# Optimization experiments

Measured on AMD Instinct MI355X. Metric: run time of the kernel, lower is better.

Reference implementation:

```python
import jax, jax.numpy as jnp
import numpy as np

TAU = 1.5
SCALE = 0.125
EPS = 1e-5
H = 8

@jax.custom_vjp
def spike(u):
    return (u >= 0.0).astype(u.dtype)

def _spike_fwd(u):
    return spike(u), u

def _spike_bwd(u, g):
    # ATan surrogate gradient, alpha=2 (spikingjelly default)
    return (g / (1.0 + (jnp.pi * u) ** 2),)

spike.defvjp(_spike_fwd, _spike_bwd)

def lif_ms(xt):
    # xt: (T, ...) multi-step LIF, decay_input=True, v_th=1, hard reset to 0, detach_reset
    def step(v, x):
        v = v + (x - v) / TAU
        s = spike(v - 1.0)
        v = v * (1.0 - jax.lax.stop_gradient(s))
        return v, s
    _, s = jax.lax.scan(step, jnp.zeros_like(xt[0]), xt)
    return s

def bn(x, g, b, m, var):
    # eval-mode BatchNorm1d over channel dim of (B, C, L)
    inv = g / jnp.sqrt(var + EPS)
    return (x - m[None, :, None]) * inv[None, :, None] + b[None, :, None]

def setup_inputs() -> dict:
    key = jax.random.key(0)
    ks = jax.random.split(key, 16)
    B, C, T, N = 8, 512, 4, 256
    w_scale = 1.0 / np.sqrt(C)
    inp = {
        'x': jax.random.normal(ks[0], (B, C, T, N), jnp.float32),
        'wq': jax.random.normal(ks[1], (C, C), jnp.float32) * w_scale,
        'wk': jax.random.normal(ks[2], (C, C), jnp.float32) * w_scale,
        'wv': jax.random.normal(ks[3], (C, C), jnp.float32) * w_scale,
        'wp': jax.random.normal(ks[4], (C, C), jnp.float32) * w_scale,
        'bp': jnp.zeros((C,), jnp.float32),
        'gq': jax.random.uniform(ks[5], (C,), jnp.float32, 0.5, 1.5),
        'bq': jax.random.uniform(ks[6], (C,), jnp.float32),
        'mq': jnp.zeros((C,), jnp.float32),
        'vq': jnp.ones((C,), jnp.float32),
        'gk': jax.random.uniform(ks[7], (C,), jnp.float32, 0.5, 1.5),
        'bk': jax.random.uniform(ks[8], (C,), jnp.float32),
        'mk': jnp.zeros((C,), jnp.float32),
        'vk': jnp.ones((C,), jnp.float32),
        'gv': jax.random.uniform(ks[9], (C,), jnp.float32, 0.5, 1.5),
        'bv': jax.random.uniform(ks[10], (C,), jnp.float32),
        'mv': jnp.zeros((C,), jnp.float32),
        'vv': jnp.ones((C,), jnp.float32),
        'gp': jax.random.uniform(ks[11], (C,), jnp.float32, 0.5, 1.5),
        'bpn': jax.random.uniform(ks[12], (C,), jnp.float32),
        'mp': jnp.zeros((C,), jnp.float32),
        'vp': jnp.ones((C,), jnp.float32),
    }
    return inp

def reference(x, wq, wk, wv, wp, bp, gq, bq, mq, vq, gk, bk, mk, vk,
              gv, bv, mv, vv, gp, bpn, mp, vp):
    B, C, T, N = x.shape
    L = T * N
    d = C // H

    # proj_bn then multi-step proj_lif over time dim
    xb = bn(x.reshape(B, C, L), gp, bpn, mp, vp).reshape(B, C, T, N)
    s0 = lif_ms(jnp.transpose(xb, (2, 0, 1, 3)))            # (T,B,C,N)
    x_for_qkv = jnp.transpose(s0, (1, 2, 0, 3)).reshape(B, C, L)  # (B,C,L)

    def qkv_branch(w, g, b_, m, v_):
        y = bn(jnp.einsum('oc,bcl->bol', w, x_for_qkv), g, b_, m, v_)
        y = y.reshape(B, C, T, N)
        sy = lif_ms(jnp.transpose(y, (2, 0, 1, 3)))         # (T,B,C,N)
        sy = jnp.transpose(sy, (1, 0, 3, 2)).reshape(B, L, C)  # (B,T,N,C)->(B,L,C)
        return jnp.transpose(sy.reshape(B, L, H, d), (0, 2, 1, 3))  # (B,H,L,d)

    q = qkv_branch(wq, gq, bq, mq, vq)
    k = qkv_branch(wk, gk, bk, mk, vk)
    v = qkv_branch(wv, gv, bv, mv, vv)

    attn = jnp.einsum('bhqd,bhkd->bhqk', q, k)              # no softmax
    o = jnp.einsum('bhqk,bhkd->bhqd', attn, v) * SCALE
    o = jnp.transpose(o, (0, 1, 3, 2)).reshape(B, C, L)

    # single-step attn_lif: v = o/tau from zero state, spike at threshold 1
    s = spike(o / TAU - 1.0)

    out = jnp.einsum('oc,bcl->bol', wp, s) + bp[None, :, None]
    return out.reshape(B, C, T, N)
```

## Files before the change

kernel.cpp:

```cpp
#include <hip/hip_runtime.h>
#include <hip/hip_bf16.h>


#define NB 8
#define NC 512
#define NT 4
#define NN 256
#define NL 1024
#define NH 8
#define ND 64
#define BCL (NB*NC*NL)

typedef __attribute__((ext_vector_type(8))) short  short8v;
typedef __attribute__((ext_vector_type(8))) unsigned short us8;
typedef __attribute__((ext_vector_type(4))) unsigned short us4;
typedef __attribute__((ext_vector_type(4))) float f32x4;

__device__ __forceinline__ float bu2f(unsigned short u) {
  return __uint_as_float(((unsigned)u) << 16);
}
__device__ __forceinline__ unsigned short f2bu(float f) {
  unsigned b = __float_as_uint(f);
  return (unsigned short)((b + 0x7FFFu + ((b >> 16) & 1u)) >> 16);
}

__global__ void k_prep(const float* __restrict__ wq, const float* __restrict__ wk,
                       const float* __restrict__ wv, const float* __restrict__ wp,
                       const float* __restrict__ x,
                       const float* __restrict__ g,  const float* __restrict__ bt,
                       const float* __restrict__ mu, const float* __restrict__ var,
                       unsigned short* __restrict__ H2,
                       unsigned short* __restrict__ ST0) {
  if (blockIdx.x < 512) {
    int gi = blockIdx.x * 256 + threadIdx.x;
    int p = gi >> 15;
    int o = (gi >> 6) & 511;
    int k8 = gi & 63;
    int rt = o >> 7, r = o & 127;
    int k0i = k8 >> 3, chunk = k8 & 7;
    const float* W = (p == 0) ? wq : (p == 1) ? wk : (p == 2) ? wv : wp;
    const float* src = W + (size_t)o * NC + k8 * 8;
    us8 a[3];
#pragma unroll
    for (int i = 0; i < 8; i++) {
      float w = src[i];
      unsigned short u1 = f2bu(w);
      float r1 = w - bu2f(u1);
      unsigned short u2 = f2bu(r1);
      float r2 = r1 - bu2f(u2);
      unsigned short u3 = f2bu(r2);
      a[0][i] = u1; a[1][i] = u2; a[2][i] = u3;
    }
#pragma unroll
    for (int j = 0; j < 3; j++) {
      size_t off = ((size_t)((((p * 3 + j) * 4 + rt) * 8 + k0i) * 8 + chunk)) * 1024
                   + (size_t)r * 8;
      *(us8*)&H2[off] = a[j];
    }
  } else {
    int bidx = blockIdx.x - 512;
    int b  = bidx >> 6;
    int c0 = (bidx & 63) * 8;
    int n  = threadIdx.x;
    unsigned short spk[NT][8];
#pragma unroll
    for (int i = 0; i < 8; i++) {
      int c = c0 + i;
      float inv = g[c] / sqrtf(var[c] + 1e-5f);
      float m = mu[c], be = bt[c];
      const float* xp = x + ((size_t)(b * NC + c)) * NL + n;
      float v = 0.f;
#pragma unroll
      for (int t = 0; t < NT; t++) {
        float y = (xp[t * NN] - m) * inv + be;
        v = v + (y - v) / 1.5f;
        unsigned short s = 0;
        if (v - 1.0f >= 0.f) { s = 0x3F80; v = 0.f; }
        spk[t][i] = s;
      }
    }
#pragma unroll
    for (int t = 0; t < NT; t++) {
      us8 pk;
#pragma unroll
      for (int i = 0; i < 8; i++) pk[i] = spk[t][i];
      *(us8*)&ST0[((size_t)b * NL + t * NN + n) * NC + c0] = pk;
    }
  }
}

__global__ __launch_bounds__(256) void
k_qkv(const unsigned short* __restrict__ H2,
      const unsigned short* __restrict__ ST0,
      const float* __restrict__ gq, const float* __restrict__ bq,
      const float* __restrict__ mq, const float* __restrict__ vq,
      const float* __restrict__ gk, const float* __restrict__ bk,
      const float* __restrict__ mk, const float* __restrict__ vk,
      const float* __restrict__ gv, const float* __restrict__ bv,
      const float* __restrict__ mv, const float* __restrict__ vv,
      unsigned short* __restrict__ STq, unsigned short* __restrict__ STk,
      unsigned short* __restrict__ STv) {
  __shared__ __align__(16) unsigned short sB[2][128 * 64];

  int id = blockIdx.x;
  int n0 = (id & 7) * 32;
  int rt = (id >> 3) & 3;
  int b  = (id >> 5) & 7;
  int p  = id >> 8;

  int tid = threadIdx.x;
  int w = tid >> 6, lane = tid & 63, quad = lane >> 4, l15 = lane & 15;
  int xorv = l15 & 7;

  const unsigned short* Sb = ST0 + (size_t)b * NL * NC;

  f32x4 acc[2][8];
#pragma unroll
  for (int ri = 0; ri < 2; ri++)
#pragma unroll
    for (int jj = 0; jj < 8; jj++) acc[ri][jj] = (f32x4){0.f, 0.f, 0.f, 0.f};

  us8 breg[4];
  int ccs[4], segs[4];
  size_t bsrc[4];
#pragma unroll
  for (int i = 0; i < 4; i++) {
    int idx = tid + i * 256;
    int cc = idx >> 3, seg = idx & 7;
    int t = (cc >> 4) & 3, nn = (cc & 15) | ((cc >> 6) << 4);
    ccs[i] = cc; segs[i] = seg;
    bsrc[i] = (size_t)(t * NN + n0 + nn) * NC + seg * 8;
  }
#pragma unroll
  for (int i = 0; i < 4; i++) breg[i] = *(const us8*)&Sb[bsrc[i]];
#pragma unroll
  for (int i = 0; i < 4; i++)
    *(us8*)&sB[0][ccs[i] * 64 + ((segs[i] ^ (ccs[i] & 7)) << 3)] = breg[i];

  for (int k0i = 0; k0i < 8; k0i++) {
    __syncthreads();
    int buf = k0i & 1;
    if (k0i < 7) {
#pragma unroll
      for (int i = 0; i < 4; i++)
        breg[i] = *(const us8*)&Sb[bsrc[i] + (size_t)(k0i + 1) * 64];
    }
#pragma unroll
    for (int ks = 0; ks < 2; ks++) {
      int c8 = ks * 4 + quad;
      int poff = (c8 ^ xorv) << 3;
      short8v bf[8];
#pragma unroll
      for (int jj = 0; jj < 8; jj++)
        bf[jj] = *(const short8v*)&sB[buf][(jj * 16 + l15) * 64 + poff];
#pragma unroll
      for (int j = 0; j < 3; j++) {
        const unsigned short* Hj =
            H2 + ((size_t)(((p * 3 + j) * 4 + rt) * 8 + k0i)) * 8192
               + (size_t)c8 * 1024;
        short8v a0 = *(const short8v*)&Hj[(w * 32 + l15) * 8];
        short8v a1 = *(const short8v*)&Hj[(w * 32 + 16 + l15) * 8];
#pragma unroll
        for (int jj = 0; jj < 8; jj++) {
          acc[0][jj] = __builtin_amdgcn_mfma_f32_16x16x32_bf16(a0, bf[jj], acc[0][jj], 0, 0, 0);
          acc[1][jj] = __builtin_amdgcn_mfma_f32_16x16x32_bf16(a1, bf[jj], acc[1][jj], 0, 0, 0);
        }
      }
    }
    if (k0i < 7) {
#pragma unroll
      for (int i = 0; i < 4; i++)
        *(us8*)&sB[buf ^ 1][ccs[i] * 64 + ((segs[i] ^ (ccs[i] & 7)) << 3)] = breg[i];
    }
  }

  const float *g, *bb, *mm, *vr;
  unsigned short* So;
  if (p == 0)      { g = gq; bb = bq; mm = mq; vr = vq; So = STq; }
  else if (p == 1) { g = gk; bb = bk; mm = mk; vr = vk; So = STk; }
  else             { g = gv; bb = bv; mm = mv; vr = vv; So = STv; }
  So += (size_t)b * NL * NC;

#pragma unroll
  for (int ri = 0; ri < 2; ri++) {
    int ob = rt * 128 + w * 32 + ri * 16 + quad * 4;
    float av[4], mvv[4], bvv[4];
#pragma unroll
    for (int r = 0; r < 4; r++) {
      av[r]  = g[ob + r] / sqrtf(vr[ob + r] + 1e-5f);
      mvv[r] = mm[ob + r];
      bvv[r] = bb[ob + r];
    }
#pragma unroll
    for (int nh = 0; nh < 2; nh++) {
      int n = n0 + (nh << 4) + l15;
      unsigned short sp[4][4];
#pragma unroll
      for (int r = 0; r < 4; r++) {
        float vmem = 0.f;
#pragma unroll
        for (int t = 0; t < NT; t++) {
          float y = (acc[ri][nh * 4 + t][r] - mvv[r]) * av[r] + bvv[r];
          vmem = vmem + (y - vmem) / 1.5f;
          unsigned short s = 0;
          if (vmem - 1.0f >= 0.f) { s = 0x3F80; vmem = 0.f; }
          sp[t][r] = s;
        }
      }
#pragma unroll
      for (int t = 0; t < NT; t++) {
        us4 pk;
#pragma unroll
        for (int r = 0; r < 4; r++) pk[r] = sp[t][r];
        *(us4*)&So[(size_t)(t * NN + n) * NC + ob] = pk;
      }
    }
  }
}

__global__ void k_kvM(const unsigned short* __restrict__ STk,
                      const unsigned short* __restrict__ STv,
                      float* __restrict__ Mpart) {
  int bh = blockIdx.x, ch = blockIdx.y;
  int b = bh >> 3, h = bh & 7;
  const unsigned short* Kp = STk + (size_t)b * NL * NC + h * ND;
  const unsigned short* Vp = STv + (size_t)b * NL * NC + h * ND;
  __shared__ float sK[64][72];
  __shared__ float sV[64][72];
  int tid = threadIdx.x, tx = tid & 15, ty = tid >> 4;
  float acc[4][4] = {};
  for (int lt = 0; lt < 4; lt++) {
    int lb = ch * 256 + lt * 64;
#pragma unroll
    for (int i = 0; i < 2; i++) {
      int idx = tid + i * 256;
      int r = idx >> 3, seg = idx & 7;
      us8 kv = *(const us8*)&Kp[(size_t)(lb + r) * NC + seg * 8];
      us8 vv = *(const us8*)&Vp[(size_t)(lb + r) * NC + seg * 8];
#pragma unroll
      for (int q2 = 0; q2 < 8; q2++) {
        sK[r][seg * 8 + q2] = bu2f(kv[q2]);
        sV[r][seg * 8 + q2] = bu2f(vv[q2]);
      }
    }
    __syncthreads();
#pragma unroll 8
    for (int lc = 0; lc < 64; lc++) {
      float kvx[4], vvx[4];
#pragma unroll
      for (int i = 0; i < 4; i++) kvx[i] = sK[lc][ty * 4 + i];
#pragma unroll
      for (int j2 = 0; j2 < 4; j2++) vvx[j2] = sV[lc][tx * 4 + j2];
#pragma unroll
      for (int i = 0; i < 4; i++)
#pragma unroll
        for (int j2 = 0; j2 < 4; j2++)
          acc[i][j2] += kvx[i] * vvx[j2];
    }
    __syncthreads();
  }
  float* Mp = Mpart + ((size_t)ch * 64 + bh) * 4096;
#pragma unroll
  for (int i = 0; i < 4; i++) {
    float4 v4 = make_float4(acc[i][0], acc[i][1], acc[i][2], acc[i][3]);
    *(float4*)&Mp[(ty * 4 + i) * ND + tx * 4] = v4;
  }
}

__global__ void k_attn(const unsigned short* __restrict__ STq,
                       const float* __restrict__ Mpart,
                       unsigned short* __restrict__ STs) {
  int lt = blockIdx.x, bh = blockIdx.y;
  int b = bh >> 3, h = bh & 7;
  __shared__ float sM[64][64];
  __shared__ float sQT[64][65];
  int tid = threadIdx.x, tx = tid & 15, ty = tid >> 4;
#pragma unroll
  for (int i = 0; i < 16; i++) {
    int idx = tid + i * 256;
    float s = 0.f;
#pragma unroll
    for (int ch = 0; ch < 4; ch++)
      s += Mpart[((size_t)ch * 64 + bh) * 4096 + idx];
    ((float*)sM)[idx] = s;
  }
  const unsigned short* Qp = STq + (size_t)b * NL * NC + h * ND;
#pragma unroll
  for (int i = 0; i < 2; i++) {
    int idx = tid + i * 256;
    int r = idx >> 3, seg = idx & 7;
    us8 qv = *(const us8*)&Qp[(size_t)(lt * 64 + r) * NC + seg * 8];
#pragma unroll
    for (int e2 = 0; e2 < 8; e2++) sQT[seg * 8 + e2][r] = bu2f(qv[e2]);
  }
  __syncthreads();
  float acc[4][4] = {};
#pragma unroll 8
  for (int e = 0; e < 64; e++) {
    float q[4], m[4];
#pragma unroll
    for (int i = 0; i < 4; i++) q[i] = sQT[e][ty * 4 + i];
#pragma unroll
    for (int j2 = 0; j2 < 4; j2++) m[j2] = sM[e][tx * 4 + j2];
#pragma unroll
    for (int i = 0; i < 4; i++)
#pragma unroll
      for (int j2 = 0; j2 < 4; j2++)
        acc[i][j2] += q[i] * m[j2];
  }
  unsigned short* Sp = STs + (size_t)b * NL * NC + h * ND;
#pragma unroll
  for (int i = 0; i < 4; i++) {
    us4 pk;
#pragma unroll
    for (int j2 = 0; j2 < 4; j2++) pk[j2] = (acc[i][j2] >= 12.0f) ? 0x3F80 : 0;
    *(us4*)&Sp[(size_t)(lt * 64 + ty * 4 + i) * NC + tx * 4] = pk;
  }
}

__global__ __launch_bounds__(256) void
k_out(const unsigned short* __restrict__ H2,
      const unsigned short* __restrict__ STs,
      const float* __restrict__ bp, float* __restrict__ out) {
  __shared__ __align__(16) unsigned short sB[2][64 * 64];

  int id = blockIdx.x;
  int l0 = (id & 15) * 64;
  int rt = (id >> 4) & 3;
  int b  = id >> 6;

  int tid = threadIdx.x;
  int w = tid >> 6, lane = tid & 63, quad = lane >> 4, l15 = lane & 15;
  int xorv = l15 & 7;

  const unsigned short* Sb = STs + (size_t)b * NL * NC;

  f32x4 acc[2][4];
#pragma unroll
  for (int ri = 0; ri < 2; ri++)
#pragma unroll
    for (int jj = 0; jj < 4; jj++) acc[ri][jj] = (f32x4){0.f, 0.f, 0.f, 0.f};

  us8 breg[2];
  int ccs[2], segs[2];
  size_t bsrc[2];
#pragma unroll
  for (int i = 0; i < 2; i++) {
    int idx = tid + i * 256;
    int cc = idx >> 3, seg = idx & 7;
    ccs[i] = cc; segs[i] = seg;
    bsrc[i] = (size_t)(l0 + cc) * NC + seg * 8;
  }
#pragma unroll
  for (int i = 0; i < 2; i++) breg[i] = *(const us8*)&Sb[bsrc[i]];
#pragma unroll
  for (int i = 0; i < 2; i++)
    *(us8*)&sB[0][ccs[i] * 64 + ((segs[i] ^ (ccs[i] & 7)) << 3)] = breg[i];

  for (int k0i = 0; k0i < 8; k0i++) {
    __syncthreads();
    int buf = k0i & 1;
    if (k0i < 7) {
#pragma unroll
      for (int i = 0; i < 2; i++)
        breg[i] = *(const us8*)&Sb[bsrc[i] + (size_t)(k0i + 1) * 64];
    }
#pragma unroll
    for (int ks = 0; ks < 2; ks++) {
      int c8 = ks * 4 + quad;
      int poff = (c8 ^ xorv) << 3;
      short8v bf[4];
#pragma unroll
      for (int jj = 0; jj < 4; jj++)
        bf[jj] = *(const short8v*)&sB[buf][(jj * 16 + l15) * 64 + poff];
#pragma unroll
      for (int j = 0; j < 3; j++) {
        const unsigned short* Hj =
            H2 + ((size_t)(((9 + j) * 4 + rt) * 8 + k0i)) * 8192
               + (size_t)c8 * 1024;
        short8v a0 = *(const short8v*)&Hj[(w * 32 + l15) * 8];
        short8v a1 = *(const short8v*)&Hj[(w * 32 + 16 + l15) * 8];
#pragma unroll
        for (int jj = 0; jj < 4; jj++) {
          acc[0][jj] = __builtin_amdgcn_mfma_f32_16x16x32_bf16(a0, bf[jj], acc[0][jj], 0, 0, 0);
          acc[1][jj] = __builtin_amdgcn_mfma_f32_16x16x32_bf16(a1, bf[jj], acc[1][jj], 0, 0, 0);
        }
      }
    }
    if (k0i < 7) {
#pragma unroll
      for (int i = 0; i < 2; i++)
        *(us8*)&sB[buf ^ 1][ccs[i] * 64 + ((segs[i] ^ (ccs[i] & 7)) << 3)] = breg[i];
    }
  }

#pragma unroll
  for (int ri = 0; ri < 2; ri++) {
    int ob = rt * 128 + w * 32 + ri * 16 + quad * 4;
#pragma unroll
    for (int jj = 0; jj < 4; jj++) {
      int l = l0 + jj * 16 + l15;
#pragma unroll
      for (int r = 0; r < 4; r++)
        out[((size_t)(b * NC + ob + r)) * NL + l] = acc[ri][jj][r] + bp[ob + r];
    }
  }
}

extern "C" void kernel_launch(void* const* d_in, const int* in_sizes, int n_in,
                              void* d_out, int out_size, void* d_ws, size_t ws_size,
                              hipStream_t stream) {
  (void)in_sizes; (void)n_in; (void)out_size; (void)ws_size;
  const float* x   = (const float*)d_in[0];
  const float* wq  = (const float*)d_in[1];
  const float* wk  = (const float*)d_in[2];
  const float* wv  = (const float*)d_in[3];
  const float* wp  = (const float*)d_in[4];
  const float* bp  = (const float*)d_in[5];
  const float* gq  = (const float*)d_in[6];
  const float* bq  = (const float*)d_in[7];
  const float* mq  = (const float*)d_in[8];
  const float* vq  = (const float*)d_in[9];
  const float* gk  = (const float*)d_in[10];
  const float* bk  = (const float*)d_in[11];
  const float* mk  = (const float*)d_in[12];
  const float* vk  = (const float*)d_in[13];
  const float* gv  = (const float*)d_in[14];
  const float* bv  = (const float*)d_in[15];
  const float* mv  = (const float*)d_in[16];
  const float* vvv = (const float*)d_in[17];
  const float* gp  = (const float*)d_in[18];
  const float* bpn = (const float*)d_in[19];
  const float* mp  = (const float*)d_in[20];
  const float* vp  = (const float*)d_in[21];

  unsigned short* H2  = (unsigned short*)d_ws;
  unsigned short* ST0 = H2 + (size_t)4 * 3 * NC * NC;
  unsigned short* STq = ST0 + BCL;
  unsigned short* STk = STq + BCL;
  unsigned short* STv = STk + BCL;
  unsigned short* STs = STv + BCL;
  float* Mpart = (float*)(STs + BCL);

  dim3 blk(256);
  k_prep<<<1024, blk, 0, stream>>>(wq, wk, wv, wp, x, gp, bpn, mp, vp, H2, ST0);
  k_qkv<<<768, blk, 0, stream>>>(H2, ST0,
      gq, bq, mq, vq, gk, bk, mk, vk, gv, bv, mv, vvv, STq, STk, STv);
  k_kvM<<<dim3(64, 4), blk, 0, stream>>>(STk, STv, Mpart);
  k_attn<<<dim3(16, 64), blk, 0, stream>>>(STq, Mpart, STs);
  k_out<<<512, blk, 0, stream>>>(H2, STs, bp, (float*)d_out);
}
```

Measured before the change: 198.5 us.

## Move Q·M attention product to bf16 MFMA with hi/lo split and finer KV partials

The k_attn kernel is rewritten. Instead of a scalar fp32 outer-product loop, it uses 16x16x32 bf16 MFMA instructions. M is stored in LDS as a swizzled transpose, split into bf16 high and low parts, which keeps the spike threshold comparison accurate. Each block now covers 256 rows instead of 64. k_kvM is split into 8 L-chunks instead of 4 for more parallelism, and k_attn sums the 8 partials. The goal is to replace slow FMA-bound work with matrix cores, at the cost of a doubled Mpart buffer and an extra reduction pass.

```diff
diff --git a/kernel.cpp b/kernel.cpp
--- a/kernel.cpp
+++ b/kernel.cpp
@@ -229,8 +229,8 @@
   __shared__ float sV[64][72];
   int tid = threadIdx.x, tx = tid & 15, ty = tid >> 4;
   float acc[4][4] = {};
-  for (int lt = 0; lt < 4; lt++) {
-    int lb = ch * 256 + lt * 64;
+  for (int lt = 0; lt < 2; lt++) {
+    int lb = ch * 128 + lt * 64;
 #pragma unroll
     for (int i = 0; i < 2; i++) {
       int idx = tid + i * 256;
@@ -267,55 +267,85 @@
   }
 }
 
-__global__ void k_attn(const unsigned short* __restrict__ STq,
-                       const float* __restrict__ Mpart,
-                       unsigned short* __restrict__ STs) {
+__global__ __launch_bounds__(256) void
+k_attn(const unsigned short* __restrict__ STq,
+       const float* __restrict__ Mpart,
+       unsigned short* __restrict__ STs) {
+  __shared__ unsigned short MT1[64 * 64];
+  __shared__ unsigned short MT2[64 * 64];
   int lt = blockIdx.x, bh = blockIdx.y;
   int b = bh >> 3, h = bh & 7;
-  __shared__ float sM[64][64];
-  __shared__ float sQT[64][65];
-  int tid = threadIdx.x, tx = tid & 15, ty = tid >> 4;
-#pragma unroll
-  for (int i = 0; i < 16; i++) {
-    int idx = tid + i * 256;
-    float s = 0.f;
-#pragma unroll
-    for (int ch = 0; ch < 4; ch++)
-      s += Mpart[((size_t)ch * 64 + bh) * 4096 + idx];
-    ((float*)sM)[idx] = s;
-  }
+  int tid = threadIdx.x;
+  int w = tid >> 6, lane = tid & 63, quad = lane >> 4, l15 = lane & 15;
+
+#pragma unroll
+  for (int i = 0; i < 4; i++) {
+    int idx4 = tid + i * 256;
+    float4 s = ((const float4*)Mpart)[(size_t)bh * 1024 + idx4];
+#pragma unroll
+    for (int ch = 1; ch < 8; ch++) {
+      float4 t = ((const float4*)Mpart)[((size_t)ch * 64 + bh) * 1024 + idx4];
+      s.x += t.x; s.y += t.y; s.z += t.z; s.w += t.w;
+    }
+    int e = idx4 >> 4;
+    int dd0 = (idx4 * 4) & 63;
+    int chunk = e >> 3;
+    float sv[4] = {s.x, s.y, s.z, s.w};
+#pragma unroll
+    for (int r = 0; r < 4; r++) {
+      int dd = dd0 + r;
+      unsigned short u1 = f2bu(sv[r]);
+      unsigned short u2 = f2bu(sv[r] - bu2f(u1));
+      int pos = dd * 64 + (((chunk ^ (dd & 7)) << 3) | (e & 7));
+      MT1[pos] = u1;
+      MT2[pos] = u2;
+    }
+  }
+  __syncthreads();
+
   const unsigned short* Qp = STq + (size_t)b * NL * NC + h * ND;
-#pragma unroll
-  for (int i = 0; i < 2; i++) {
-    int idx = tid + i * 256;
-    int r = idx >> 3, seg = idx & 7;
-    us8 qv = *(const us8*)&Qp[(size_t)(lt * 64 + r) * NC + seg * 8];
-#pragma unroll
-    for (int e2 = 0; e2 < 8; e2++) sQT[seg * 8 + e2][r] = bu2f(qv[e2]);
-  }
-  __syncthreads();
-  float acc[4][4] = {};
-#pragma unroll 8
-  for (int e = 0; e < 64; e++) {
-    float q[4], m[4];
-#pragma unroll
-    for (int i = 0; i < 4; i++) q[i] = sQT[e][ty * 4 + i];
-#pragma unroll
-    for (int j2 = 0; j2 < 4; j2++) m[j2] = sM[e][tx * 4 + j2];
-#pragma unroll
-    for (int i = 0; i < 4; i++)
-#pragma unroll
-      for (int j2 = 0; j2 < 4; j2++)
-        acc[i][j2] += q[i] * m[j2];
-  }
+  int lbase = lt * 256 + w * 64;
+
+  f32x4 acc[4][4];
+#pragma unroll
+  for (int dt = 0; dt < 4; dt++)
+#pragma unroll
+    for (int j = 0; j < 4; j++) acc[dt][j] = (f32x4){0.f, 0.f, 0.f, 0.f};
+
+#pragma unroll
+  for (int ks = 0; ks < 2; ks++) {
+    short8v bq[4];
+#pragma unroll
+    for (int ltile = 0; ltile < 4; ltile++)
+      bq[ltile] = *(const short8v*)&Qp[(size_t)(lbase + ltile * 16 + l15) * NC
+                                       + ks * 32 + quad * 8];
+    int c8 = ks * 4 + quad;
+#pragma unroll
+    for (int dt = 0; dt < 4; dt++) {
+      int dd = dt * 16 + l15;
+      int off = dd * 64 + ((c8 ^ (dd & 7)) << 3);
+      short8v a1 = *(const short8v*)&MT1[off];
+      short8v a2 = *(const short8v*)&MT2[off];
+#pragma unroll
+      for (int ltile = 0; ltile < 4; ltile++) {
+        acc[dt][ltile] = __builtin_amdgcn_mfma_f32_16x16x32_bf16(a1, bq[ltile], acc[dt][ltile], 0, 0, 0);
+        acc[dt][ltile] = __builtin_amdgcn_mfma_f32_16x16x32_bf16(a2, bq[ltile], acc[dt][ltile], 0, 0, 0);
+      }
+    }
+  }
+
   unsigned short* Sp = STs + (size_t)b * NL * NC + h * ND;
 #pragma unroll
-  for (int i = 0; i < 4; i++) {
-    us4 pk;
-#pragma unroll
-    for (int j2 = 0; j2 < 4; j2++) pk[j2] = (acc[i][j2] >= 12.0f) ? 0x3F80 : 0;
-    *(us4*)&Sp[(size_t)(lt * 64 + ty * 4 + i) * NC + tx * 4] = pk;
-  }
+  for (int dt = 0; dt < 4; dt++)
+#pragma unroll
+    for (int ltile = 0; ltile < 4; ltile++) {
+      int l = lbase + ltile * 16 + l15;
+      int dd = dt * 16 + quad * 4;
+      us4 pk;
+#pragma unroll
+      for (int r = 0; r < 4; r++) pk[r] = (acc[dt][ltile][r] >= 12.0f) ? 0x3F80 : 0;
+      *(us4*)&Sp[(size_t)l * NC + dd] = pk;
+    }
 }
 
 __global__ __launch_bounds__(256) void
@@ -446,7 +476,7 @@
   k_prep<<<1024, blk, 0, stream>>>(wq, wk, wv, wp, x, gp, bpn, mp, vp, H2, ST0);
   k_qkv<<<768, blk, 0, stream>>>(H2, ST0,
       gq, bq, mq, vq, gk, bk, mk, vk, gv, bv, mv, vvv, STq, STk, STv);
-  k_kvM<<<dim3(64, 4), blk, 0, stream>>>(STk, STv, Mpart);
-  k_attn<<<dim3(16, 64), blk, 0, stream>>>(STq, Mpart, STs);
+  k_kvM<<<dim3(64, 8), blk, 0, stream>>>(STk, STv, Mpart);
+  k_attn<<<dim3(4, 64), blk, 0, stream>>>(STq, Mpart, STs);
   k_out<<<512, blk, 0, stream>>>(H2, STs, bp, (float*)d_out);
 }
```

Result: no change. 198.8 us (+0.2%).
